# Kernel tuning notes

Measured on AMD Instinct MI355X. Metric: run time of the kernel, lower is better.

## Reference

```python
import jax, jax.numpy as jnp
import numpy as np

N = 4096
RANK = 4
B = 2048
DT = 1.0
TAU = 1.0
ALPHA = float(np.sqrt(np.pi) / 2.0)  # erf slope so phi'(0)=1


def setup_inputs() -> dict:
    key = jax.random.key(0)
    k1, k2, k3, k4, k5, k6 = jax.random.split(key, 6)
    return {
        "x_t": jax.random.normal(k1, (1, B), dtype=jnp.float32),
        "h": jax.random.normal(k2, (N, B), dtype=jnp.float32),
        "m": jax.random.normal(k3, (N, 1), dtype=jnp.float32),
        "u": jax.random.normal(k4, (N, RANK), dtype=jnp.float32),
        "v": jax.random.normal(k5, (N, RANK), dtype=jnp.float32),
        "z": jax.random.normal(k6, (N, 1), dtype=jnp.float32),
    }


def reference(x_t, h, m, u, v, z):
    # phi(h) = erf(alpha * h)
    phi_h = jax.lax.erf(ALPHA * h)                      # [N, B]
    # W @ phi_h with W = (1/N) u v^T, reassociated to exploit low rank
    # (mathematically identical to materializing W)
    wph = (u @ (v.T @ phi_h)) / N                       # [N, B]
    h_update = wph + m @ x_t                            # [N, B]
    h_new = h + (DT / TAU) * (-h + h_update)            # [N, B]
    y = (z.T @ phi_h) / N                               # [1, B]
    return (y, h_new)
```

## Files before the change

kernel.cpp:

```cpp
#include <hip/hip_runtime.h>
#include <math.h>

#define N 4096
#define B 2048
#define RANK 4
#define ALPHA 0.8862269254527580f
#define INV_N (1.0f / 4096.0f)

#define RPB1 8
#define SPLITS (N / RPB1)
#define P (5 * B)
#define STRIPE 64
#define GRP 8
#define SPG (SPLITS / GRP)
#define RPB3 4

typedef float vf4 __attribute__((ext_vector_type(4)));

__device__ __forceinline__ float erf_fast(float t) {
  const float A = 0.140012288f;
  const float FP = 1.2732395447f;
  float t2 = t * t;
  float num = fmaf(A, t2, FP);
  float den = fmaf(A, t2, 1.0f);
  float r = t2 * num * __builtin_amdgcn_rcpf(den);
  float e = __expf(-r);
  float s = __builtin_amdgcn_sqrtf(fmaxf(1.0f - e, 0.0f));
  return copysignf(s, t);
}

__global__ __launch_bounds__(512) void k_reduce_partial(
    const float* __restrict__ h, const float* __restrict__ v,
    const float* __restrict__ z, float* __restrict__ partials) {
  const int tid = threadIdx.x;
  const int row0 = blockIdx.x * RPB1;

  vf4 a0 = {0.f, 0.f, 0.f, 0.f};
  vf4 a1 = a0, a2 = a0, a3 = a0, a4 = a0;

  const float* hp = h + (size_t)row0 * B + tid * 4;
#pragma unroll
  for (int r = 0; r < RPB1; ++r) {
    const vf4 hv = *(const vf4*)(hp + (size_t)r * B);
    vf4 p;
    p.x = erf_fast(ALPHA * hv.x);
    p.y = erf_fast(ALPHA * hv.y);
    p.z = erf_fast(ALPHA * hv.z);
    p.w = erf_fast(ALPHA * hv.w);
    const float v0 = v[(row0 + r) * RANK + 0];
    const float v1 = v[(row0 + r) * RANK + 1];
    const float v2 = v[(row0 + r) * RANK + 2];
    const float v3 = v[(row0 + r) * RANK + 3];
    const float zr = z[row0 + r];
    a0.x = fmaf(v0, p.x, a0.x); a0.y = fmaf(v0, p.y, a0.y);
    a0.z = fmaf(v0, p.z, a0.z); a0.w = fmaf(v0, p.w, a0.w);
    a1.x = fmaf(v1, p.x, a1.x); a1.y = fmaf(v1, p.y, a1.y);
    a1.z = fmaf(v1, p.z, a1.z); a1.w = fmaf(v1, p.w, a1.w);
    a2.x = fmaf(v2, p.x, a2.x); a2.y = fmaf(v2, p.y, a2.y);
    a2.z = fmaf(v2, p.z, a2.z); a2.w = fmaf(v2, p.w, a2.w);
    a3.x = fmaf(v3, p.x, a3.x); a3.y = fmaf(v3, p.y, a3.y);
    a3.z = fmaf(v3, p.z, a3.z); a3.w = fmaf(v3, p.w, a3.w);
    a4.x = fmaf(zr, p.x, a4.x); a4.y = fmaf(zr, p.y, a4.y);
    a4.z = fmaf(zr, p.z, a4.z); a4.w = fmaf(zr, p.w, a4.w);
  }

  float* pp = partials + (size_t)blockIdx.x * P + tid * 4;
  *(vf4*)(pp + 0 * B) = a0;
  *(vf4*)(pp + 1 * B) = a1;
  *(vf4*)(pp + 2 * B) = a2;
  *(vf4*)(pp + 3 * B) = a3;
  *(vf4*)(pp + 4 * B) = a4;
}

__global__ __launch_bounds__(512) void k_reduce_final(
    const float* __restrict__ partials, float* __restrict__ sfin,
    float* __restrict__ y) {
  __shared__ float red[GRP][STRIPE];
  const int c = threadIdx.x & (STRIPE - 1);
  const int g = threadIdx.x >> 6;
  const int f0 = blockIdx.x * STRIPE;
  const float* pp = partials + (size_t)(g * SPG) * P + f0 + c;
  float ssum = 0.f;
#pragma unroll 8
  for (int sp = 0; sp < SPG; ++sp)
    ssum += pp[(size_t)sp * P];
  red[g][c] = ssum;
  __syncthreads();
  if (threadIdx.x < STRIPE) {
    float tot = 0.f;
#pragma unroll
    for (int g2 = 0; g2 < GRP; ++g2)
      tot += red[g2][threadIdx.x];
    const int f = f0 + threadIdx.x;
    if (f < RANK * B)
      sfin[f] = tot;
    else
      y[f - RANK * B] = tot * INV_N;
  }
}

__global__ __launch_bounds__(256) void k_update(
    const float* __restrict__ sfin, const float* __restrict__ u,
    const float* __restrict__ m, const float* __restrict__ x,
    float* __restrict__ hnew) {
  const int tid = threadIdx.x;
  const int row0 = blockIdx.x * RPB3;
  const int c0 = tid * 4;

  const vf4 sA0 = *(const vf4*)(sfin + 0 * B + c0);
  const vf4 sA1 = *(const vf4*)(sfin + 1 * B + c0);
  const vf4 sA2 = *(const vf4*)(sfin + 2 * B + c0);
  const vf4 sA3 = *(const vf4*)(sfin + 3 * B + c0);
  const vf4 xa  = *(const vf4*)(x + c0);
  const vf4 sB0 = *(const vf4*)(sfin + 0 * B + c0 + 1024);
  const vf4 sB1 = *(const vf4*)(sfin + 1 * B + c0 + 1024);
  const vf4 sB2 = *(const vf4*)(sfin + 2 * B + c0 + 1024);
  const vf4 sB3 = *(const vf4*)(sfin + 3 * B + c0 + 1024);
  const vf4 xb  = *(const vf4*)(x + c0 + 1024);

  float* op = hnew + (size_t)row0 * B + c0;
#pragma unroll
  for (int i = 0; i < RPB3; ++i) {
    const int n = row0 + i;
    const vf4 uv = *(const vf4*)(u + (size_t)n * RANK);
    const float mv = m[n];
    vf4 oA, oB;
    oA.x = fmaf(mv, xa.x,
                (sA0.x * uv.x + sA1.x * uv.y + sA2.x * uv.z + sA3.x * uv.w) * INV_N);
    oA.y = fmaf(mv, xa.y,
                (sA0.y * uv.x + sA1.y * uv.y + sA2.y * uv.z + sA3.y * uv.w) * INV_N);
    oA.z = fmaf(mv, xa.z,
                (sA0.z * uv.x + sA1.z * uv.y + sA2.z * uv.z + sA3.z * uv.w) * INV_N);
    oA.w = fmaf(mv, xa.w,
                (sA0.w * uv.x + sA1.w * uv.y + sA2.w * uv.z + sA3.w * uv.w) * INV_N);
    oB.x = fmaf(mv, xb.x,
                (sB0.x * uv.x + sB1.x * uv.y + sB2.x * uv.z + sB3.x * uv.w) * INV_N);
    oB.y = fmaf(mv, xb.y,
                (sB0.y * uv.x + sB1.y * uv.y + sB2.y * uv.z + sB3.y * uv.w) * INV_N);
    oB.z = fmaf(mv, xb.z,
                (sB0.z * uv.x + sB1.z * uv.y + sB2.z * uv.z + sB3.z * uv.w) * INV_N);
    oB.w = fmaf(mv, xb.w,
                (sB0.w * uv.x + sB1.w * uv.y + sB2.w * uv.z + sB3.w * uv.w) * INV_N);
    __builtin_nontemporal_store(oA, (vf4*)(op + (size_t)i * B));
    __builtin_nontemporal_store(oB, (vf4*)(op + (size_t)i * B + 1024));
  }
}

extern "C" void kernel_launch(void* const* d_in, const int* in_sizes, int n_in,
                              void* d_out, int out_size, void* d_ws,
                              size_t ws_size, hipStream_t stream) {
  const float* x = (const float*)d_in[0];
  const float* h = (const float*)d_in[1];
  const float* m = (const float*)d_in[2];
  const float* u = (const float*)d_in[3];
  const float* v = (const float*)d_in[4];
  const float* z = (const float*)d_in[5];

  float* y = (float*)d_out;
  float* hnew = (float*)d_out + B;

  float* partials = (float*)d_ws;
  float* sfin = partials + (size_t)SPLITS * P;

  k_reduce_partial<<<SPLITS, 512, 0, stream>>>(h, v, z, partials);
  k_reduce_final<<<P / STRIPE, 512, 0, stream>>>(partials, sfin, y);
  k_update<<<N / RPB3, 256, 0, stream>>>(sfin, u, m, x, hnew);
}
```

Baseline: 106.2 us.

## Replace two-stage partial reduction with float atomics into a zeroed accumulator

The per-block partial sums used to be written to a large workspace (512 blocks x 5B floats) and reduced by a separate kernel. Now each block atomically adds its 5x2048 partials into a single zeroed accumulator, and the update kernel also writes y. This removes roughly 20 MB of partial-buffer writes and re-reads plus one reduction kernel, in exchange for a tiny zeroing kernel and heavy atomic contention: 512 blocks hit the same 10K addresses. Summation order is no longer deterministic.

```diff
diff --git a/kernel.cpp b/kernel.cpp
--- a/kernel.cpp
+++ b/kernel.cpp
@@ -8,11 +8,8 @@
 #define INV_N (1.0f / 4096.0f)
 
 #define RPB1 8
-#define SPLITS (N / RPB1)
-#define P (5 * B)
-#define STRIPE 64
-#define GRP 8
-#define SPG (SPLITS / GRP)
+#define NBLK1 (N / RPB1)
+#define ACCSZ (5 * B)
 #define RPB3 4
 
 typedef float vf4 __attribute__((ext_vector_type(4)));
@@ -29,9 +26,13 @@
   return copysignf(s, t);
 }
 
+__global__ __launch_bounds__(512) void k_zero(float* __restrict__ acc) {
+  acc[blockIdx.x * 512 + threadIdx.x] = 0.f;
+}
+
 __global__ __launch_bounds__(512) void k_reduce_partial(
     const float* __restrict__ h, const float* __restrict__ v,
-    const float* __restrict__ z, float* __restrict__ partials) {
+    const float* __restrict__ z, float* __restrict__ acc) {
   const int tid = threadIdx.x;
   const int row0 = blockIdx.x * RPB1;
 
@@ -64,58 +65,53 @@
     a4.z = fmaf(zr, p.z, a4.z); a4.w = fmaf(zr, p.w, a4.w);
   }
 
-  float* pp = partials + (size_t)blockIdx.x * P + tid * 4;
-  *(vf4*)(pp + 0 * B) = a0;
-  *(vf4*)(pp + 1 * B) = a1;
-  *(vf4*)(pp + 2 * B) = a2;
-  *(vf4*)(pp + 3 * B) = a3;
-  *(vf4*)(pp + 4 * B) = a4;
-}
-
-__global__ __launch_bounds__(512) void k_reduce_final(
-    const float* __restrict__ partials, float* __restrict__ sfin,
-    float* __restrict__ y) {
-  __shared__ float red[GRP][STRIPE];
-  const int c = threadIdx.x & (STRIPE - 1);
-  const int g = threadIdx.x >> 6;
-  const int f0 = blockIdx.x * STRIPE;
-  const float* pp = partials + (size_t)(g * SPG) * P + f0 + c;
-  float ssum = 0.f;
-#pragma unroll 8
-  for (int sp = 0; sp < SPG; ++sp)
-    ssum += pp[(size_t)sp * P];
-  red[g][c] = ssum;
-  __syncthreads();
-  if (threadIdx.x < STRIPE) {
-    float tot = 0.f;
-#pragma unroll
-    for (int g2 = 0; g2 < GRP; ++g2)
-      tot += red[g2][threadIdx.x];
-    const int f = f0 + threadIdx.x;
-    if (f < RANK * B)
-      sfin[f] = tot;
-    else
-      y[f - RANK * B] = tot * INV_N;
-  }
+  const int c0 = tid * 4;
+  unsafeAtomicAdd(acc + 0 * B + c0 + 0, a0.x);
+  unsafeAtomicAdd(acc + 0 * B + c0 + 1, a0.y);
+  unsafeAtomicAdd(acc + 0 * B + c0 + 2, a0.z);
+  unsafeAtomicAdd(acc + 0 * B + c0 + 3, a0.w);
+  unsafeAtomicAdd(acc + 1 * B + c0 + 0, a1.x);
+  unsafeAtomicAdd(acc + 1 * B + c0 + 1, a1.y);
+  unsafeAtomicAdd(acc + 1 * B + c0 + 2, a1.z);
+  unsafeAtomicAdd(acc + 1 * B + c0 + 3, a1.w);
+  unsafeAtomicAdd(acc + 2 * B + c0 + 0, a2.x);
+  unsafeAtomicAdd(acc + 2 * B + c0 + 1, a2.y);
+  unsafeAtomicAdd(acc + 2 * B + c0 + 2, a2.z);
+  unsafeAtomicAdd(acc + 2 * B + c0 + 3, a2.w);
+  unsafeAtomicAdd(acc + 3 * B + c0 + 0, a3.x);
+  unsafeAtomicAdd(acc + 3 * B + c0 + 1, a3.y);
+  unsafeAtomicAdd(acc + 3 * B + c0 + 2, a3.z);
+  unsafeAtomicAdd(acc + 3 * B + c0 + 3, a3.w);
+  unsafeAtomicAdd(acc + 4 * B + c0 + 0, a4.x);
+  unsafeAtomicAdd(acc + 4 * B + c0 + 1, a4.y);
+  unsafeAtomicAdd(acc + 4 * B + c0 + 2, a4.z);
+  unsafeAtomicAdd(acc + 4 * B + c0 + 3, a4.w);
 }
 
 __global__ __launch_bounds__(256) void k_update(
-    const float* __restrict__ sfin, const float* __restrict__ u,
+    const float* __restrict__ acc, const float* __restrict__ u,
     const float* __restrict__ m, const float* __restrict__ x,
-    float* __restrict__ hnew) {
+    float* __restrict__ hnew, float* __restrict__ y) {
   const int tid = threadIdx.x;
   const int row0 = blockIdx.x * RPB3;
   const int c0 = tid * 4;
 
-  const vf4 sA0 = *(const vf4*)(sfin + 0 * B + c0);
-  const vf4 sA1 = *(const vf4*)(sfin + 1 * B + c0);
-  const vf4 sA2 = *(const vf4*)(sfin + 2 * B + c0);
-  const vf4 sA3 = *(const vf4*)(sfin + 3 * B + c0);
+  if (blockIdx.x == 0) {
+    const vf4 t0 = *(const vf4*)(acc + 4 * B + c0);
+    const vf4 t1 = *(const vf4*)(acc + 4 * B + c0 + 1024);
+    *(vf4*)(y + c0) = t0 * INV_N;
+    *(vf4*)(y + c0 + 1024) = t1 * INV_N;
+  }
+
+  const vf4 sA0 = *(const vf4*)(acc + 0 * B + c0);
+  const vf4 sA1 = *(const vf4*)(acc + 1 * B + c0);
+  const vf4 sA2 = *(const vf4*)(acc + 2 * B + c0);
+  const vf4 sA3 = *(const vf4*)(acc + 3 * B + c0);
   const vf4 xa  = *(const vf4*)(x + c0);
-  const vf4 sB0 = *(const vf4*)(sfin + 0 * B + c0 + 1024);
-  const vf4 sB1 = *(const vf4*)(sfin + 1 * B + c0 + 1024);
-  const vf4 sB2 = *(const vf4*)(sfin + 2 * B + c0 + 1024);
-  const vf4 sB3 = *(const vf4*)(sfin + 3 * B + c0 + 1024);
+  const vf4 sB0 = *(const vf4*)(acc + 0 * B + c0 + 1024);
+  const vf4 sB1 = *(const vf4*)(acc + 1 * B + c0 + 1024);
+  const vf4 sB2 = *(const vf4*)(acc + 2 * B + c0 + 1024);
+  const vf4 sB3 = *(const vf4*)(acc + 3 * B + c0 + 1024);
   const vf4 xb  = *(const vf4*)(x + c0 + 1024);
 
   float* op = hnew + (size_t)row0 * B + c0;
@@ -159,10 +155,9 @@
   float* y = (float*)d_out;
   float* hnew = (float*)d_out + B;
 
-  float* partials = (float*)d_ws;
-  float* sfin = partials + (size_t)SPLITS * P;
+  float* acc = (float*)d_ws;
 
-  k_reduce_partial<<<SPLITS, 512, 0, stream>>>(h, v, z, partials);
-  k_reduce_final<<<P / STRIPE, 512, 0, stream>>>(partials, sfin, y);
-  k_update<<<N / RPB3, 256, 0, stream>>>(sfin, u, m, x, hnew);
+  k_zero<<<ACCSZ / 512, 512, 0, stream>>>(acc);
+  k_reduce_partial<<<NBLK1, 512, 0, stream>>>(h, v, z, acc);
+  k_update<<<N / RPB3, 256, 0, stream>>>(acc, u, m, x, hnew, y);
 }
```

Result: slower. 222.6 us (+109.5%).
